# Kernel tuning notes

Hardware: AMD Instinct MI355X
Metric: run time of the kernel (lower is better)

Reference implementation:

```python
import jax, jax.numpy as jnp
import numpy as np

B, S, D = 1, 2048, 4096
H, KVH, HD = 32, 8, 128
ROPE_THETA = 10000.0


def setup_inputs() -> dict:
    key = jax.random.key(0)
    k1, k2, k3, k4, k5 = jax.random.split(key, 5)
    scale = D ** -0.5
    return {
        "hidden_states": jax.random.normal(k1, (B, S, D), dtype=jnp.float32),
        "position_ids": jnp.arange(S, dtype=jnp.int64).reshape(1, S),
        "Wq": jax.random.normal(k2, (H * HD, D), dtype=jnp.float32) * scale,
        "Wk": jax.random.normal(k3, (KVH * HD, D), dtype=jnp.float32) * scale,
        "Wv": jax.random.normal(k4, (KVH * HD, D), dtype=jnp.float32) * scale,
        "Wo": jax.random.normal(k5, (D, H * HD), dtype=jnp.float32) * scale,
    }


def _rotate_half(x):
    x1, x2 = x[..., : HD // 2], x[..., HD // 2 :]
    return jnp.concatenate((-x2, x1), axis=-1)


def reference(hidden_states, position_ids, Wq, Wk, Wv, Wo):
    b, s, d = hidden_states.shape
    # projections: nn.Linear applies x @ W.T
    q = jnp.einsum("bsd,ed->bse", hidden_states, Wq).reshape(b, s, H, HD).transpose(0, 2, 1, 3)
    k = jnp.einsum("bsd,ed->bse", hidden_states, Wk).reshape(b, s, KVH, HD).transpose(0, 2, 1, 3)
    v = jnp.einsum("bsd,ed->bse", hidden_states, Wv).reshape(b, s, KVH, HD).transpose(0, 2, 1, 3)
    # rotary embedding (default rope: inv_freq = theta^(-2i/d), attention_scaling = 1)
    inv_freq = 1.0 / (ROPE_THETA ** (jnp.arange(0, HD, 2, dtype=jnp.float32) / HD))
    pos = position_ids.astype(jnp.float32)  # [Bp, S]
    freqs = pos[:, :, None] * inv_freq[None, None, :]  # [Bp, S, HD/2]
    emb = jnp.concatenate((freqs, freqs), axis=-1)  # [Bp, S, HD]
    cos = jnp.cos(emb)[:, None, :, :]  # unsqueeze head dim
    sin = jnp.sin(emb)[:, None, :, :]
    q = q * cos + _rotate_half(q) * sin
    k = k * cos + _rotate_half(k) * sin
    # GQA: expand kv heads to match query heads
    groups = H // KVH
    k = jnp.repeat(k, groups, axis=1)
    v = jnp.repeat(v, groups, axis=1)
    # causal attention, scaling = head_dim^-0.5
    scores = jnp.einsum("bhqd,bhkd->bhqk", q, k) * (HD ** -0.5)
    causal = jnp.tril(jnp.ones((s, s), dtype=bool))
    scores = jnp.where(causal[None, None], scores, jnp.finfo(scores.dtype).min)
    attn = jax.nn.softmax(scores, axis=-1)
    out = jnp.einsum("bhqk,bhkd->bhqd", attn, v)
    out = out.transpose(0, 2, 1, 3).reshape(b, s, H * HD)
    return jnp.einsum("bse,de->bsd", out, Wo)
```

## Files before the change

kernel.cpp:

```cpp
#include <hip/hip_runtime.h>
#include <stdint.h>

typedef unsigned short u16;
typedef __attribute__((ext_vector_type(4))) float f32x4;
typedef __attribute__((ext_vector_type(8))) short bf16x8;

static constexpr int S   = 2048;
static constexpr int DM  = 4096;
static constexpr int NH  = 32;
static constexpr int NKV = 8;
static constexpr int HD  = 128;
static constexpr int LDQ = 5120;

__device__ __forceinline__ u16 f2bf(float f) {
    union { float f; unsigned u; } v; v.f = f;
    return (u16)((v.u + 0x7FFFu + ((v.u >> 16) & 1u)) >> 16);
}
__device__ __forceinline__ float bf2f(u16 h) {
    union { unsigned u; float f; } v; v.u = ((unsigned)h) << 16;
    return v.f;
}

__device__ __forceinline__ void mfma16(f32x4& d, bf16x8 a, bf16x8 b) {
    asm("v_mfma_f32_16x16x32_bf16 %0, %1, %2, %0" : "+v"(d) : "v"(a), "v"(b));
}

__device__ __forceinline__ void gload_lds16(const u16* g, u16* lds) {
    __builtin_amdgcn_global_load_lds((__attribute__((address_space(1))) void*)g,
                                     (__attribute__((address_space(3))) void*)lds,
                                     16, 0, 0);
}

__global__ __launch_bounds__(256) void cvt_kernel(const float* __restrict__ in,
                                                  u16* __restrict__ out, int n4) {
    int i = blockIdx.x * blockDim.x + threadIdx.x;
    int stride = gridDim.x * blockDim.x;
    for (; i < n4; i += stride) {
        float4 v = ((const float4*)in)[i];
        ushort4 o;
        o.x = f2bf(v.x); o.y = f2bf(v.y); o.z = f2bf(v.z); o.w = f2bf(v.w);
        ((ushort4*)out)[i] = o;
    }
}

__global__ __launch_bounds__(256) void cvt_qkv(const float* __restrict__ Wq,
                                               const float* __restrict__ Wk,
                                               const float* __restrict__ Wv,
                                               u16* __restrict__ out) {
    const int n4 = 6144 * 4096 / 4;
    int i = blockIdx.x * blockDim.x + threadIdx.x;
    int stride = gridDim.x * blockDim.x;
    for (; i < n4; i += stride) {
        float4 v;
        if (i < 4194304)       v = ((const float4*)Wq)[i];
        else if (i < 5242880)  v = ((const float4*)Wk)[i - 4194304];
        else                   v = ((const float4*)Wv)[i - 5242880];
        ushort4 o;
        o.x = f2bf(v.x); o.y = f2bf(v.y); o.z = f2bf(v.z); o.w = f2bf(v.w);
        ((ushort4*)out)[i] = o;
    }
}

__global__ __launch_bounds__(256) void rope_table_kernel(float2* __restrict__ tbl) {
    int i = blockIdx.x * blockDim.x + threadIdx.x;
    if (i >= S * 64) return;
    int p = i >> 6, j = i & 63;
    float inv = powf(10000.0f, -(float)j / 64.0f);
    float a = (float)p * inv;
    tbl[i] = make_float2(cosf(a), sinf(a));
}

__global__ __launch_bounds__(256) void rope_kernel(u16* __restrict__ X,
                                                   const float2* __restrict__ tbl,
                                                   int nh, int ld, float scale) {
    int i = blockIdx.x * blockDim.x + threadIdx.x;
    int total = S * nh * 64;
    if (i >= total) return;
    int dd = i & 63;
    int t2 = i >> 6;
    int hh = t2 % nh;
    int s  = t2 / nh;
    size_t base = (size_t)s * ld + (size_t)hh * HD + dd;
    float x1 = bf2f(X[base]);
    float x2 = bf2f(X[base + 64]);
    float2 cs = tbl[(s << 6) + dd];
    X[base]      = f2bf((x1 * cs.x - x2 * cs.y) * scale);
    X[base + 64] = f2bf((x2 * cs.x + x1 * cs.y) * scale);
}

__global__ __launch_bounds__(256)
void gemm_bt(const u16* __restrict__ A, const u16* __restrict__ Bt,
             float* __restrict__ C, int M, int N, int K, int lda, int ldb, int ldc) {
    __shared__ u16 Al[128 * 64];
    __shared__ u16 Bl[128 * 64];
    const int t = threadIdx.x;
    const int w = t >> 6, l = t & 63;
    const int r16 = l & 15, g4 = l >> 4;
    const int m0 = blockIdx.y * 128, n0 = blockIdx.x * 128;
    const int wr = (w >> 1) * 64, wc = (w & 1) * 64;

    f32x4 acc[4][4];
#pragma unroll
    for (int i = 0; i < 4; ++i)
#pragma unroll
        for (int j = 0; j < 4; ++j) acc[i][j] = f32x4{0.f, 0.f, 0.f, 0.f};

    for (int kt = 0; kt < K; kt += 64) {
#pragma unroll
        for (int i = 0; i < 4; ++i) {
            int c = i * 256 + t;
            int r = c >> 3, s = (c & 7) ^ (r & 7);
            gload_lds16(A + (size_t)(m0 + r) * lda + kt + (s << 3),
                        Al + ((i * 256 + w * 64) << 3));
        }
#pragma unroll
        for (int i = 0; i < 4; ++i) {
            int c = i * 256 + t;
            int r = c >> 3, s = (c & 7) ^ (r & 7);
            gload_lds16(Bt + (size_t)(n0 + r) * ldb + kt + (s << 3),
                        Bl + ((i * 256 + w * 64) << 3));
        }
        asm volatile("s_waitcnt vmcnt(0)" ::: "memory");
        __syncthreads();

#pragma unroll
        for (int kk = 0; kk < 2; ++kk) {
            bf16x8 af[4], bfr[4];
#pragma unroll
            for (int mi = 0; mi < 4; ++mi) {
                int r = wr + mi * 16 + r16;
                af[mi] = *(const bf16x8*)((const char*)Al +
                          ((r * 128 + kk * 64 + g4 * 16) ^ ((r & 7) << 4)));
            }
#pragma unroll
            for (int ni = 0; ni < 4; ++ni) {
                int r = wc + ni * 16 + r16;
                bfr[ni] = *(const bf16x8*)((const char*)Bl +
                           ((r * 128 + kk * 64 + g4 * 16) ^ ((r & 7) << 4)));
            }
#pragma unroll
            for (int mi = 0; mi < 4; ++mi)
#pragma unroll
                for (int ni = 0; ni < 4; ++ni)
                    mfma16(acc[mi][ni], af[mi], bfr[ni]);
        }
        __syncthreads();
    }

    const int rb = g4 * 4;
#pragma unroll
    for (int mi = 0; mi < 4; ++mi)
#pragma unroll
        for (int ni = 0; ni < 4; ++ni) {
            const int n = n0 + wc + ni * 16 + r16;
            const int mbase = m0 + wr + mi * 16 + rb;
#pragma unroll
            for (int j = 0; j < 4; ++j)
                C[(size_t)(mbase + j) * ldc + n] = acc[mi][ni][j];
        }
}

__global__ __launch_bounds__(256)
void gemm_qkv(const u16* __restrict__ A, const u16* __restrict__ Bt,
              u16* __restrict__ Cqk, u16* __restrict__ Vt) {
    __shared__ u16 Al[128 * 64];
    __shared__ u16 Bl[128 * 64];
    const int t = threadIdx.x;
    const int w = t >> 6, l = t & 63;
    const int r16 = l & 15, g4 = l >> 4;
    const int m0 = blockIdx.y * 128, n0 = blockIdx.x * 128;
    const int wr = (w >> 1) * 64, wc = (w & 1) * 64;

    f32x4 acc[4][4];
#pragma unroll
    for (int i = 0; i < 4; ++i)
#pragma unroll
        for (int j = 0; j < 4; ++j) acc[i][j] = f32x4{0.f, 0.f, 0.f, 0.f};

    for (int kt = 0; kt < DM; kt += 64) {
#pragma unroll
        for (int i = 0; i < 4; ++i) {
            int c = i * 256 + t;
            int r = c >> 3, s = (c & 7) ^ (r & 7);
            gload_lds16(A + (size_t)(m0 + r) * DM + kt + (s << 3),
                        Al + ((i * 256 + w * 64) << 3));
        }
#pragma unroll
        for (int i = 0; i < 4; ++i) {
            int c = i * 256 + t;
            int r = c >> 3, s = (c & 7) ^ (r & 7);
            gload_lds16(Bt + (size_t)(n0 + r) * DM + kt + (s << 3),
                        Bl + ((i * 256 + w * 64) << 3));
        }
        asm volatile("s_waitcnt vmcnt(0)" ::: "memory");
        __syncthreads();

#pragma unroll
        for (int kk = 0; kk < 2; ++kk) {
            bf16x8 af[4], bfr[4];
#pragma unroll
            for (int mi = 0; mi < 4; ++mi) {
                int r = wr + mi * 16 + r16;
                af[mi] = *(const bf16x8*)((const char*)Al +
                          ((r * 128 + kk * 64 + g4 * 16) ^ ((r & 7) << 4)));
            }
#pragma unroll
            for (int ni = 0; ni < 4; ++ni) {
                int r = wc + ni * 16 + r16;
                bfr[ni] = *(const bf16x8*)((const char*)Bl +
                           ((r * 128 + kk * 64 + g4 * 16) ^ ((r & 7) << 4)));
            }
#pragma unroll
            for (int mi = 0; mi < 4; ++mi)
#pragma unroll
                for (int ni = 0; ni < 4; ++ni)
                    mfma16(acc[mi][ni], af[mi], bfr[ni]);
        }
        __syncthreads();
    }

    const int rb = g4 * 4;
    if (n0 < 5120) {
#pragma unroll
        for (int mi = 0; mi < 4; ++mi)
#pragma unroll
            for (int ni = 0; ni < 4; ++ni) {
                const int n = n0 + wc + ni * 16 + r16;
                const int mbase = m0 + wr + mi * 16 + rb;
#pragma unroll
                for (int j = 0; j < 4; ++j)
                    Cqk[(size_t)(mbase + j) * LDQ + n] = f2bf(acc[mi][ni][j]);
            }
    } else {
#pragma unroll
        for (int mi = 0; mi < 4; ++mi)
#pragma unroll
            for (int ni = 0; ni < 4; ++ni) {
                const int n = n0 + wc + ni * 16 + r16 - 5120;
                const int mbase = m0 + wr + mi * 16 + rb;
                ushort4 v4;
                v4.x = f2bf(acc[mi][ni][0]); v4.y = f2bf(acc[mi][ni][1]);
                v4.z = f2bf(acc[mi][ni][2]); v4.w = f2bf(acc[mi][ni][3]);
                *(ushort4*)&Vt[(size_t)n * S + mbase] = v4;
            }
    }
}

__global__ __launch_bounds__(512, 2)
void attn_fwd(const u16* __restrict__ QK, const u16* __restrict__ Vt,
              u16* __restrict__ O) {
    __shared__ u16 Kl[2][64 * 128];
    __shared__ u16 Vl[2][128 * 64];
    __shared__ u16 Pl[8 * 16 * 64];

    const int t = threadIdx.x;
    const int w = t >> 6, l = t & 63;
    const int r16 = l & 15, g4 = l >> 4;
    const int h = blockIdx.y;
    const int kvh = h >> 2;
    const int p = blockIdx.x;
    const int q0A = p * 128, q0B = (15 - p) * 128;
    const int ntA = 2 * p + 2, ntB = 32 - 2 * p;

    const u16* Kg = QK + 4096 + kvh * HD;
    const u16* Vg = Vt + (size_t)(kvh * HD) * S;
    u16* Pb = &Pl[w * 1024];

    bf16x8 qfA[4], qfB[4];
    {
        const u16* Qg = QK + h * HD;
        const size_t qrA = (size_t)(q0A + w * 16 + r16) * LDQ;
        const size_t qrB = (size_t)(q0B + w * 16 + r16) * LDQ;
#pragma unroll
        for (int kg = 0; kg < 4; ++kg) {
            qfA[kg] = *(const bf16x8*)&Qg[qrA + kg * 32 + g4 * 8];
            qfB[kg] = *(const bf16x8*)&Qg[qrB + kg * 32 + g4 * 8];
        }
    }

    f32x4 accA[8], accB[8];
    float mA[4], lA[4], mB[4], lB[4];
#pragma unroll
    for (int i = 0; i < 8; ++i) { accA[i] = f32x4{0,0,0,0}; accB[i] = f32x4{0,0,0,0}; }
#pragma unroll
    for (int j = 0; j < 4; ++j) { mA[j] = -3.0e38f; lA[j] = 0.f; mB[j] = -3.0e38f; lB[j] = 0.f; }

    auto stage = [&](int tk, int b) {
        const int kv0 = tk * 64;
#pragma unroll
        for (int i = 0; i < 2; ++i) {
            int c = i * 512 + t;
            int r = c >> 4, s = (c & 15) ^ (r & 7);
            gload_lds16(Kg + (size_t)(kv0 + r) * LDQ + (s << 3),
                        &Kl[b][0] + ((i * 512 + w * 64) << 3));
        }
#pragma unroll
        for (int i = 0; i < 2; ++i) {
            int c = i * 512 + t;
            int r = c >> 3, s = (c & 7) ^ (r & 7);
            gload_lds16(Vg + (size_t)r * S + kv0 + (s << 3),
                        &Vl[b][0] + ((i * 512 + w * 64) << 3));
        }
    };

    auto compute = [&](f32x4 (&acco)[8], float (&mrun)[4], float (&lrun)[4],
                       const bf16x8 (&qf)[4], int q0, int tk, int b) {
        const int kv0 = tk * 64;
        const bool maskit = (kv0 + 63 > q0 + (w << 4));
        const u16* Kb = &Kl[b][0];
        const u16* Vb = &Vl[b][0];

        f32x4 sc[4];
#pragma unroll
        for (int ni = 0; ni < 4; ++ni) sc[ni] = f32x4{0,0,0,0};
        __builtin_amdgcn_s_setprio(1);
#pragma unroll
        for (int kg = 0; kg < 4; ++kg) {
#pragma unroll
            for (int ni = 0; ni < 4; ++ni) {
                int row = ni * 16 + r16;
                int bb = (row * 256 + kg * 64 + g4 * 16) ^ ((row & 7) << 4);
                bf16x8 kf = *(const bf16x8*)((const char*)Kb + bb);
                mfma16(sc[ni], qf[kg], kf);
            }
        }
        __builtin_amdgcn_s_setprio(0);

        float vmax[4];
        bool grow = false;
#pragma unroll
        for (int j = 0; j < 4; ++j) {
            if (maskit) {
                const int qg = q0 + w * 16 + g4 * 4 + j;
#pragma unroll
                for (int ni = 0; ni < 4; ++ni)
                    if (kv0 + ni * 16 + r16 > qg) sc[ni][j] = -3.0e38f;
            }
            float v = fmaxf(fmaxf(sc[0][j], sc[1][j]), fmaxf(sc[2][j], sc[3][j]));
            v = fmaxf(v, __shfl_xor(v, 1, 16));
            v = fmaxf(v, __shfl_xor(v, 2, 16));
            v = fmaxf(v, __shfl_xor(v, 4, 16));
            v = fmaxf(v, __shfl_xor(v, 8, 16));
            vmax[j] = v;
            grow = grow || (v > mrun[j] + 11.5f);
        }
        float fac[4] = {1.f, 1.f, 1.f, 1.f};
        if (__any(grow)) {
#pragma unroll
            for (int j = 0; j < 4; ++j) {
                float nm = fmaxf(mrun[j], vmax[j]);
                fac[j] = exp2f(mrun[j] - nm);
                mrun[j] = nm;
            }
#pragma unroll
            for (int i = 0; i < 8; ++i)
#pragma unroll
                for (int j = 0; j < 4; ++j) acco[i][j] *= fac[j];
        }
#pragma unroll
        for (int j = 0; j < 4; ++j) {
            float p0 = exp2f(sc[0][j] - mrun[j]);
            float p1 = exp2f(sc[1][j] - mrun[j]);
            float p2 = exp2f(sc[2][j] - mrun[j]);
            float p3 = exp2f(sc[3][j] - mrun[j]);
            sc[0][j] = p0; sc[1][j] = p1; sc[2][j] = p2; sc[3][j] = p3;
            float s2 = (p0 + p1) + (p2 + p3);
            s2 += __shfl_xor(s2, 1, 16);
            s2 += __shfl_xor(s2, 2, 16);
            s2 += __shfl_xor(s2, 4, 16);
            s2 += __shfl_xor(s2, 8, 16);
            lrun[j] = lrun[j] * fac[j] + s2;
        }

#pragma unroll
        for (int ni = 0; ni < 4; ++ni)
#pragma unroll
            for (int j = 0; j < 4; ++j) {
                int row = g4 * 4 + j;
                int bb = (row * 128 + ((ni * 16 + r16) << 1)) ^ ((row & 7) << 4);
                *(u16*)((char*)Pb + bb) = f2bf(sc[ni][j]);
            }
        asm volatile("s_waitcnt lgkmcnt(0)" ::: "memory");
        __builtin_amdgcn_sched_barrier(0);

        int pb0 = (r16 * 128 + g4 * 16) ^ ((r16 & 7) << 4);
        bf16x8 pf0 = *(const bf16x8*)((const char*)Pb + pb0);
        bf16x8 pf1 = *(const bf16x8*)((const char*)Pb + (pb0 ^ 64));
        __builtin_amdgcn_s_setprio(1);
#pragma unroll
        for (int ni = 0; ni < 8; ++ni) {
            int row = ni * 16 + r16;
            int bb = (row * 128 + g4 * 16) ^ ((row & 7) << 4);
            bf16x8 v0 = *(const bf16x8*)((const char*)Vb + bb);
            mfma16(acco[ni], pf0, v0);
            bf16x8 v1 = *(const bf16x8*)((const char*)Vb + (bb ^ 64));
            mfma16(acco[ni], pf1, v1);
        }
        __builtin_amdgcn_s_setprio(0);
    };

    auto epilogue = [&](f32x4 (&acco)[8], float (&lrun)[4], int q0) {
        float rl[4];
#pragma unroll
        for (int j = 0; j < 4; ++j) rl[j] = 1.0f / lrun[j];
#pragma unroll
        for (int ni = 0; ni < 8; ++ni)
#pragma unroll
            for (int j = 0; j < 4; ++j) {
                const int qg = q0 + w * 16 + g4 * 4 + j;
                O[(size_t)qg * DM + h * HD + ni * 16 + r16] = f2bf(acco[ni][j] * rl[j]);
            }
    };

    stage(0, 0);
    asm volatile("s_waitcnt vmcnt(0)" ::: "memory");
    __syncthreads();
    int buf = 0;

    for (int tk = 0; tk < ntB; ++tk) {
        if (tk + 1 < ntB) stage(tk + 1, buf ^ 1);
        compute(accB, mB, lB, qfB, q0B, tk, buf);
        if (tk < ntA) compute(accA, mA, lA, qfA, q0A, tk, buf);
        asm volatile("s_waitcnt vmcnt(0)" ::: "memory");
        __syncthreads();
        buf ^= 1;
    }
    epilogue(accA, lA, q0A);
    epilogue(accB, lB, q0B);
}

extern "C" void kernel_launch(void* const* d_in, const int* in_sizes, int n_in,
                              void* d_out, int out_size, void* d_ws, size_t ws_size,
                              hipStream_t stream) {
    const float* X  = (const float*)d_in[0];
    const float* Wq = (const float*)d_in[2];
    const float* Wk = (const float*)d_in[3];
    const float* Wv = (const float*)d_in[4];
    const float* Wo = (const float*)d_in[5];

    char* ws = (char*)d_ws;
    u16*    Xbf  = (u16*)(ws + 0);
    u16*    Wqkv = (u16*)(ws + 16777216);
    u16*    Wobf = (u16*)(ws + 67108864);
    u16*    QKb  = (u16*)(ws + 100663296);
    u16*    Vtbf = (u16*)(ws + 121634816);
    u16*    Obf  = (u16*)(ws + 125829120);
    float2* tbl  = (float2*)(ws + 142606336);
    if (ws_size < 143654912ull) return;

    dim3 blk(256);

    cvt_kernel<<<2048, blk, 0, stream>>>(X,  Xbf,  S * DM / 4);
    cvt_qkv<<<2048, blk, 0, stream>>>(Wq, Wk, Wv, Wqkv);
    cvt_kernel<<<2048, blk, 0, stream>>>(Wo, Wobf, DM * DM / 4);
    rope_table_kernel<<<(S * 64 + 255) / 256, blk, 0, stream>>>(tbl);

    gemm_qkv<<<dim3(48, 16), blk, 0, stream>>>(Xbf, Wqkv, QKb, Vtbf);

    rope_kernel<<<(S * NH * 64 + 255) / 256, blk, 0, stream>>>(
        QKb, tbl, NH, LDQ, 0.08838834764831845f * 1.4426950408889634f);
    rope_kernel<<<(S * NKV * 64 + 255) / 256, blk, 0, stream>>>(
        QKb + 4096, tbl, NKV, LDQ, 1.0f);

    attn_fwd<<<dim3(8, NH), dim3(512), 0, stream>>>(QKb, Vtbf, Obf);

    gemm_bt<<<dim3(DM / 128, S / 128), blk, 0, stream>>>(
        Obf, Wobf, (float*)d_out, S, DM, DM, DM, DM, DM);
}
```

Baseline: 358.2 us.

## Merge conversion and rope launches, split attention into smaller 256-thread blocks

After: 362.5 us. No clear change (+1.2%).

```diff
diff --git a/kernel.cpp b/kernel.cpp
--- a/kernel.cpp
+++ b/kernel.cpp
@@ -20,6 +20,11 @@
     union { unsigned u; float f; } v; v.u = ((unsigned)h) << 16;
     return v.f;
 }
+__device__ __forceinline__ unsigned pk2bf(float lo, float hi) {
+    unsigned r;
+    asm("v_cvt_pk_bf16_f32 %0, %1, %2" : "=v"(r) : "v"(lo), "v"(hi));
+    return r;
+}
 
 __device__ __forceinline__ void mfma16(f32x4& d, bf16x8 a, bf16x8 b) {
     asm("v_mfma_f32_16x16x32_bf16 %0, %1, %2, %0" : "+v"(d) : "v"(a), "v"(b));
@@ -31,30 +36,22 @@
                                      16, 0, 0);
 }
 
-__global__ __launch_bounds__(256) void cvt_kernel(const float* __restrict__ in,
-                                                  u16* __restrict__ out, int n4) {
-    int i = blockIdx.x * blockDim.x + threadIdx.x;
-    int stride = gridDim.x * blockDim.x;
-    for (; i < n4; i += stride) {
-        float4 v = ((const float4*)in)[i];
-        ushort4 o;
-        o.x = f2bf(v.x); o.y = f2bf(v.y); o.z = f2bf(v.z); o.w = f2bf(v.w);
-        ((ushort4*)out)[i] = o;
-    }
-}
-
-__global__ __launch_bounds__(256) void cvt_qkv(const float* __restrict__ Wq,
+__global__ __launch_bounds__(256) void cvt_all(const float* __restrict__ X,
+                                               const float* __restrict__ Wq,
                                                const float* __restrict__ Wk,
                                                const float* __restrict__ Wv,
+                                               const float* __restrict__ Wo,
                                                u16* __restrict__ out) {
-    const int n4 = 6144 * 4096 / 4;
+    const int n4 = 12582912;
     int i = blockIdx.x * blockDim.x + threadIdx.x;
     int stride = gridDim.x * blockDim.x;
     for (; i < n4; i += stride) {
         float4 v;
-        if (i < 4194304)       v = ((const float4*)Wq)[i];
-        else if (i < 5242880)  v = ((const float4*)Wk)[i - 4194304];
-        else                   v = ((const float4*)Wv)[i - 5242880];
+        if (i < 2097152)       v = ((const float4*)X)[i];
+        else if (i < 6291456)  v = ((const float4*)Wq)[i - 2097152];
+        else if (i < 7340032)  v = ((const float4*)Wk)[i - 6291456];
+        else if (i < 8388608)  v = ((const float4*)Wv)[i - 7340032];
+        else                   v = ((const float4*)Wo)[i - 8388608];
         ushort4 o;
         o.x = f2bf(v.x); o.y = f2bf(v.y); o.z = f2bf(v.z); o.w = f2bf(v.w);
         ((ushort4*)out)[i] = o;
@@ -70,17 +67,20 @@
     tbl[i] = make_float2(cosf(a), sinf(a));
 }
 
-__global__ __launch_bounds__(256) void rope_kernel(u16* __restrict__ X,
-                                                   const float2* __restrict__ tbl,
-                                                   int nh, int ld, float scale) {
+__global__ __launch_bounds__(256) void rope2_kernel(u16* __restrict__ X,
+                                                    const float2* __restrict__ tbl,
+                                                    float qscale) {
     int i = blockIdx.x * blockDim.x + threadIdx.x;
-    int total = S * nh * 64;
+    const int total = S * 40 * 64;
     if (i >= total) return;
     int dd = i & 63;
     int t2 = i >> 6;
-    int hh = t2 % nh;
-    int s  = t2 / nh;
-    size_t base = (size_t)s * ld + (size_t)hh * HD + dd;
+    int hh = t2 % 40;
+    int s  = t2 / 40;
+    size_t base;
+    float scale;
+    if (hh < 32) { base = (size_t)s * LDQ + hh * HD + dd;               scale = qscale; }
+    else         { base = (size_t)s * LDQ + 4096 + (hh - 32) * HD + dd; scale = 1.0f;   }
     float x1 = bf2f(X[base]);
     float x2 = bf2f(X[base + 64]);
     float2 cs = tbl[(s << 6) + dd];
@@ -246,12 +246,12 @@
     }
 }
 
-__global__ __launch_bounds__(512, 2)
+__global__ __launch_bounds__(256, 3)
 void attn_fwd(const u16* __restrict__ QK, const u16* __restrict__ Vt,
               u16* __restrict__ O) {
     __shared__ u16 Kl[2][64 * 128];
     __shared__ u16 Vl[2][128 * 64];
-    __shared__ u16 Pl[8 * 16 * 64];
+    __shared__ u16 Pl[4 * 16 * 64];
 
     const int t = threadIdx.x;
     const int w = t >> 6, l = t & 63;
@@ -259,8 +259,8 @@
     const int h = blockIdx.y;
     const int kvh = h >> 2;
     const int p = blockIdx.x;
-    const int q0A = p * 128, q0B = (15 - p) * 128;
-    const int ntA = 2 * p + 2, ntB = 32 - 2 * p;
+    const int q0A = p * 64, q0B = (31 - p) * 64;
+    const int ntA = p + 1, ntB = 32 - p;
 
     const u16* Kg = QK + 4096 + kvh * HD;
     const u16* Vg = Vt + (size_t)(kvh * HD) * S;
@@ -288,25 +288,24 @@
     auto stage = [&](int tk, int b) {
         const int kv0 = tk * 64;
 #pragma unroll
-        for (int i = 0; i < 2; ++i) {
-            int c = i * 512 + t;
+        for (int i = 0; i < 4; ++i) {
+            int c = i * 256 + t;
             int r = c >> 4, s = (c & 15) ^ (r & 7);
             gload_lds16(Kg + (size_t)(kv0 + r) * LDQ + (s << 3),
-                        &Kl[b][0] + ((i * 512 + w * 64) << 3));
-        }
-#pragma unroll
-        for (int i = 0; i < 2; ++i) {
-            int c = i * 512 + t;
+                        &Kl[b][0] + ((i * 256 + w * 64) << 3));
+        }
+#pragma unroll
+        for (int i = 0; i < 4; ++i) {
+            int c = i * 256 + t;
             int r = c >> 3, s = (c & 7) ^ (r & 7);
             gload_lds16(Vg + (size_t)r * S + kv0 + (s << 3),
-                        &Vl[b][0] + ((i * 512 + w * 64) << 3));
+                        &Vl[b][0] + ((i * 256 + w * 64) << 3));
         }
     };
 
     auto compute = [&](f32x4 (&acco)[8], float (&mrun)[4], float (&lrun)[4],
-                       const bf16x8 (&qf)[4], int q0, int tk, int b) {
+                       const bf16x8 (&qf)[4], int q0, int tk, bool maskit, int b) {
         const int kv0 = tk * 64;
-        const bool maskit = (kv0 + 63 > q0 + (w << 4));
         const u16* Kb = &Kl[b][0];
         const u16* Vb = &Vl[b][0];
 
@@ -372,14 +371,20 @@
             lrun[j] = lrun[j] * fac[j] + s2;
         }
 
-#pragma unroll
-        for (int ni = 0; ni < 4; ++ni)
-#pragma unroll
-            for (int j = 0; j < 4; ++j) {
-                int row = g4 * 4 + j;
-                int bb = (row * 128 + ((ni * 16 + r16) << 1)) ^ ((row & 7) << 4);
-                *(u16*)((char*)Pb + bb) = f2bf(sc[ni][j]);
-            }
+        {
+            char* pp = (char*)Pb;
+            const int rb_ = g4 * 4;
+#pragma unroll
+            for (int ni = 0; ni < 4; ++ni) {
+                unsigned r01 = pk2bf(sc[ni][0], sc[ni][1]);
+                unsigned r23 = pk2bf(sc[ni][2], sc[ni][3]);
+                const int col2 = (ni * 16 + r16) << 1;
+                *(u16*)(pp + (((rb_ + 0) * 128 + col2) ^ (((rb_ + 0) & 7) << 4))) = (u16)r01;
+                *(u16*)(pp + (((rb_ + 1) * 128 + col2) ^ (((rb_ + 1) & 7) << 4))) = (u16)(r01 >> 16);
+                *(u16*)(pp + (((rb_ + 2) * 128 + col2) ^ (((rb_ + 2) & 7) << 4))) = (u16)r23;
+                *(u16*)(pp + (((rb_ + 3) * 128 + col2) ^ (((rb_ + 3) & 7) << 4))) = (u16)(r23 >> 16);
+            }
+        }
         asm volatile("s_waitcnt lgkmcnt(0)" ::: "memory");
         __builtin_amdgcn_sched_barrier(0);
 
@@ -419,8 +424,8 @@
 
     for (int tk = 0; tk < ntB; ++tk) {
         if (tk + 1 < ntB) stage(tk + 1, buf ^ 1);
-        compute(accB, mB, lB, qfB, q0B, tk, buf);
-        if (tk < ntA) compute(accA, mA, lA, qfA, q0A, tk, buf);
+        compute(accB, mB, lB, qfB, q0B, tk, tk == ntB - 1, buf);
+        if (tk < ntA) compute(accA, mA, lA, qfA, q0A, tk, tk == ntA - 1, buf);
         asm volatile("s_waitcnt vmcnt(0)" ::: "memory");
         __syncthreads();
         buf ^= 1;
@@ -450,19 +455,15 @@
 
     dim3 blk(256);
 
-    cvt_kernel<<<2048, blk, 0, stream>>>(X,  Xbf,  S * DM / 4);
-    cvt_qkv<<<2048, blk, 0, stream>>>(Wq, Wk, Wv, Wqkv);
-    cvt_kernel<<<2048, blk, 0, stream>>>(Wo, Wobf, DM * DM / 4);
+    cvt_all<<<2048, blk, 0, stream>>>(X, Wq, Wk, Wv, Wo, (u16*)ws);
     rope_table_kernel<<<(S * 64 + 255) / 256, blk, 0, stream>>>(tbl);
 
     gemm_qkv<<<dim3(48, 16), blk, 0, stream>>>(Xbf, Wqkv, QKb, Vtbf);
 
-    rope_kernel<<<(S * NH * 64 + 255) / 256, blk, 0, stream>>>(
-        QKb, tbl, NH, LDQ, 0.08838834764831845f * 1.4426950408889634f);
-    rope_kernel<<<(S * NKV * 64 + 255) / 256, blk, 0, stream>>>(
-        QKb + 4096, tbl, NKV, LDQ, 1.0f);
-
-    attn_fwd<<<dim3(8, NH), dim3(512), 0, stream>>>(QKb, Vtbf, Obf);
+    rope2_kernel<<<(S * 40 * 64 + 255) / 256, blk, 0, stream>>>(
+        QKb, tbl, 0.08838834764831845f * 1.4426950408889634f);
+
+    attn_fwd<<<dim3(16, NH), blk, 0, stream>>>(QKb, Vtbf, Obf);
 
     gemm_bt<<<dim3(DM / 128, S / 128), blk, 0, stream>>>(
         Obf, Wobf, (float*)d_out, S, DM, DM, DM, DM, DM);
```
